# Kernel tuning notes

Measured on AMD Instinct MI355X. Metric: run time of the kernel, lower is better.

The kernel has to match this reference:

```python
import jax, jax.numpy as jnp
import numpy as np

INPUT_DIM = 512
HIDDEN_DIM = 512


def _linear_params(key, in_dim, out_dim):
    kw, kb = jax.random.split(key)
    bound = 1.0 / np.sqrt(in_dim)
    W = jax.random.uniform(kw, (out_dim, in_dim), minval=-bound, maxval=bound, dtype=jnp.float32)
    b = jax.random.uniform(kb, (out_dim,), minval=-bound, maxval=bound, dtype=jnp.float32)
    return W, b


def setup_inputs() -> dict:
    key = jax.random.key(0)
    keys = jax.random.split(key, 11)
    B = 8192
    inp = {
        "x_t": jax.random.normal(keys[0], (B, INPUT_DIM), dtype=jnp.float32),
        "h_tm1": jax.random.normal(keys[1], (B, HIDDEN_DIM), dtype=jnp.float32),
        "c_tm1": jax.random.normal(keys[2], (B, HIDDEN_DIM), dtype=jnp.float32),
    }
    names = ["f_x", "f_h", "i_x", "i_h", "g_x", "g_h", "o_x", "o_h"]
    for n, k in zip(names, keys[3:]):
        in_dim = INPUT_DIM if n.endswith("_x") else HIDDEN_DIM
        W, b = _linear_params(k, in_dim, HIDDEN_DIM)
        inp[f"W_{n}"] = W
        inp[f"b_{n}"] = b
    return inp


def reference(x_t, h_tm1, c_tm1,
              W_f_x, b_f_x, W_f_h, b_f_h,
              W_i_x, b_i_x, W_i_h, b_i_h,
              W_g_x, b_g_x, W_g_h, b_g_h,
              W_o_x, b_o_x, W_o_h, b_o_h):
    # Stacked weights: [4, H, D] -> einsum over D gives [B, 4, H].
    Wx = jnp.stack([W_f_x, W_g_x, W_i_x, W_o_x])  # [4, H, Din]
    bx = jnp.stack([b_f_x, b_g_x, b_i_x, b_o_x])  # [4, H]
    Wh = jnp.stack([W_f_h, W_g_h, W_i_h, W_o_h])
    bh = jnp.stack([b_f_h, b_g_h, b_i_h, b_o_h])
    pre = (jnp.einsum('bd,ghd->bgh', x_t, Wx) + bx
           + jnp.einsum('bd,ghd->bgh', h_tm1, Wh) + bh)  # [B, 4, H]
    f_t = jax.nn.sigmoid(pre[:, 0])
    g_t = jnp.tanh(pre[:, 1])
    i_t = jax.nn.sigmoid(pre[:, 2])
    o_t = jax.nn.sigmoid(pre[:, 3])
    c_t = f_t * c_tm1 + i_t * g_t
    h_t = o_t * jnp.tanh(c_t)
    return (h_t, c_t)
```

## Files before the change

kernel.cpp:

```cpp
#include <hip/hip_runtime.h>
#include <cstdint>
#include <cstddef>


typedef __attribute__((ext_vector_type(8))) short short8;
typedef __attribute__((ext_vector_type(4))) float floatx4;

#define AS1(p) ((const __attribute__((address_space(1))) void*)(p))
#define AS3(p) ((__attribute__((address_space(3))) void*)(p))

__device__ __forceinline__ unsigned short f2bf(float f) {
  union { float f; unsigned u; } v; v.f = f;
  unsigned u = v.u;
  return (unsigned short)((u + 0x7fffu + ((u >> 16) & 1u)) >> 16);
}

struct PackArgs {
  const float* x; const float* h;
  const float* wx[4]; const float* wh[4];
  const float* bx[4]; const float* bh[4];
  unsigned short* A; unsigned short* B; float* bias;
};

__global__ __launch_bounds__(256) void pack_all_kernel(PackArgs P) {
  const int bid = blockIdx.x;
  if (bid < 8192) {
    int e = (bid * 256 + threadIdx.x) * 4;
    int b = e >> 10, k = e & 1023;
    const float* src = (k < 512) ? (P.x + b * 512 + k)
                                 : (P.h + b * 512 + (k - 512));
    float4 v = *(const float4*)src;
    ushort4 o;
    o.x = f2bf(v.x); o.y = f2bf(v.y); o.z = f2bf(v.z); o.w = f2bf(v.w);
    *(ushort4*)(P.A + e) = o;
  } else {
    int e = ((bid - 8192) * 256 + threadIdx.x) * 4;
    int n = e >> 10, k = e & 1023;
    int g = n & 3, hh = n >> 2;
    const float* src = (k < 512) ? (P.wx[g] + hh * 512 + k)
                                 : (P.wh[g] + hh * 512 + (k - 512));
    float4 v = *(const float4*)src;
    ushort4 o;
    o.x = f2bf(v.x); o.y = f2bf(v.y); o.z = f2bf(v.z); o.w = f2bf(v.w);
    *(ushort4*)(P.B + e) = o;
    if (k == 0) P.bias[n] = P.bx[g][hh] + P.bh[g][hh];
  }
}

__global__ __launch_bounds__(256, 4)
void lstm_gemm_kernel(const unsigned short* __restrict__ A,
                      const unsigned short* __restrict__ B,
                      const float* __restrict__ bias,
                      const float* __restrict__ c_prev,
                      float* __restrict__ h_out,
                      float* __restrict__ c_out) {
  __shared__ __align__(16) char smem[33792];
  __shared__ __align__(16) float biasS[128];

  const int tid  = threadIdx.x;
  const int lane = tid & 63;
  const int w    = tid >> 6;
  const int quad = lane >> 4;
  const int colA = lane & 15;
  const int m0   = blockIdx.x * 128;
  const int n0   = blockIdx.y * 128;
  const int h0   = blockIdx.y * 32;

  if (tid < 128) biasS[tid] = bias[n0 + tid];

  const int wm = (w >> 1) * 64;
  const int wn = (w & 1) * 64;

  const int srow = tid >> 3;
  const int cl   = tid & 7;
  const int cg   = cl ^ (srow & 7);

  floatx4 acc[4][4];
#pragma unroll
  for (int i = 0; i < 4; ++i)
#pragma unroll
    for (int j = 0; j < 4; ++j) acc[i][j] = (floatx4){0.f, 0.f, 0.f, 0.f};

  const char* Ag = (const char*)A;
  const char* Bg = (const char*)B;

  for (int kt = 0; kt < 16; ++kt) {
    __syncthreads();
    const int kb = kt * 128;
#pragma unroll
    for (int j = 0; j < 4; ++j) {
      int r = j * 32 + srow;
      __builtin_amdgcn_global_load_lds(
          AS1(Ag + (size_t)(m0 + r) * 2048 + kb + cg * 16),
          AS3(smem + r * 128 + cl * 16), 16, 0, 0);
    }
#pragma unroll
    for (int j = 0; j < 4; ++j) {
      int r = j * 32 + srow;
      __builtin_amdgcn_global_load_lds(
          AS1(Bg + (size_t)(n0 + r) * 2048 + kb + cg * 16),
          AS3(smem + 16384 + r * 128 + cl * 16), 16, 0, 0);
    }
    __syncthreads();

#pragma unroll
    for (int kk = 0; kk < 2; ++kk) {
      const int off = ((kk * 4 + quad) ^ (colA & 7)) * 16;
      short8 af[4], bfr[4];
#pragma unroll
      for (int mi = 0; mi < 4; ++mi)
        af[mi] = *(const short8*)(smem + (wm + mi * 16 + colA) * 128 + off);
#pragma unroll
      for (int ni = 0; ni < 4; ++ni)
        bfr[ni] = *(const short8*)(smem + 16384 + (wn + ni * 16 + colA) * 128 + off);
#pragma unroll
      for (int mi = 0; mi < 4; ++mi)
#pragma unroll
        for (int ni = 0; ni < 4; ++ni)
          acc[mi][ni] = __builtin_amdgcn_mfma_f32_16x16x32_bf16(
              af[mi], bfr[ni], acc[mi][ni], 0, 0, 0);
    }
  }

  __syncthreads();
  float* ep = (float*)smem;
#pragma unroll
  for (int rd = 0; rd < 2; ++rd) {
    float cp[8];
#pragma unroll
    for (int j = 0; j < 8; ++j) {
      int idx  = j * 256 + tid;
      int mloc = idx >> 5;
      int hh   = idx & 31;
      cp[j] = c_prev[(m0 + rd * 64 + mloc) * 512 + h0 + hh];
    }
    if ((w >> 1) == rd) {
#pragma unroll
      for (int mi = 0; mi < 4; ++mi)
#pragma unroll
        for (int ni = 0; ni < 4; ++ni) {
          int rr0 = mi * 16 + quad * 4;
          int cc  = wn + ni * 16 + colA;
#pragma unroll
          for (int rr = 0; rr < 4; ++rr)
            ep[(rr0 + rr) * 132 + cc] = acc[mi][ni][rr];
        }
    }
    __syncthreads();
#pragma unroll
    for (int j = 0; j < 8; ++j) {
      int idx  = j * 256 + tid;
      int mloc = idx >> 5;
      int hh   = idx & 31;
      float4 pre = *(const float4*)(ep + mloc * 132 + hh * 4);
      float4 bb  = *(const float4*)(biasS + hh * 4);
      float pf = pre.x + bb.x;
      float pi = pre.y + bb.y;
      float pg = pre.z + bb.z;
      float po = pre.w + bb.w;
      float fg = 1.f / (1.f + __expf(-pf));
      float ig = 1.f / (1.f + __expf(-pi));
      float gg = 1.f - 2.f / (1.f + __expf(2.f * pg));
      float og = 1.f / (1.f + __expf(-po));
      float cv = fg * cp[j] + ig * gg;
      float th = 1.f - 2.f / (1.f + __expf(2.f * cv));
      int m  = m0 + rd * 64 + mloc;
      int hg = h0 + hh;
      h_out[m * 512 + hg] = og * th;
      c_out[m * 512 + hg] = cv;
    }
    __syncthreads();
  }
}

extern "C" void kernel_launch(void* const* d_in, const int* in_sizes, int n_in,
                              void* d_out, int out_size, void* d_ws, size_t ws_size,
                              hipStream_t stream) {
  char* ws = (char*)d_ws;
  unsigned short* Abf = (unsigned short*)ws;
  unsigned short* Bbf = (unsigned short*)(ws + (size_t)16777216);
  float* bias = (float*)(ws + (size_t)16777216 + 4194304);

  float* hout = (float*)d_out;
  float* cout = hout + (size_t)8192 * 512;

  PackArgs P;
  P.x = (const float*)d_in[0];
  P.h = (const float*)d_in[1];
  P.wx[0] = (const float*)d_in[3];  P.bx[0] = (const float*)d_in[4];
  P.wh[0] = (const float*)d_in[5];  P.bh[0] = (const float*)d_in[6];
  P.wx[1] = (const float*)d_in[7];  P.bx[1] = (const float*)d_in[8];
  P.wh[1] = (const float*)d_in[9];  P.bh[1] = (const float*)d_in[10];
  P.wx[2] = (const float*)d_in[11]; P.bx[2] = (const float*)d_in[12];
  P.wh[2] = (const float*)d_in[13]; P.bh[2] = (const float*)d_in[14];
  P.wx[3] = (const float*)d_in[15]; P.bx[3] = (const float*)d_in[16];
  P.wh[3] = (const float*)d_in[17]; P.bh[3] = (const float*)d_in[18];
  P.A = Abf; P.B = Bbf; P.bias = bias;

  pack_all_kernel<<<10240, 256, 0, stream>>>(P);

  const float* c = (const float*)d_in[2];
  dim3 grid(64, 16);
  lstm_gemm_kernel<<<grid, 256, 0, stream>>>(Abf, Bbf, bias, c, hout, cout);
}
```

Before: 170.4 us.

## Fuse activation bf16 conversion into GEMM, loading fp32 x/h directly into LDS

Drops the separate pass that converted x and h to a bf16 concatenated buffer. The GEMM now streams fp32 activations straight from x and h_in into LDS and converts them to bf16 in registers with v_cvt_pk_bf16_f32 before the MFMAs. The block tile grows to 256x128 with 512 threads and 80KB of LDS, and only the weights are still packed. This removes a 32MB read plus 16MB write round trip, but doubles A-tile LDS traffic, adds conversion ALU work in the inner loop, and may lower occupancy.

```diff
diff --git a/kernel.cpp b/kernel.cpp
--- a/kernel.cpp
+++ b/kernel.cpp
@@ -15,104 +15,106 @@
   return (unsigned short)((u + 0x7fffu + ((u >> 16) & 1u)) >> 16);
 }
 
-struct PackArgs {
-  const float* x; const float* h;
+struct PackBArgs {
   const float* wx[4]; const float* wh[4];
   const float* bx[4]; const float* bh[4];
-  unsigned short* A; unsigned short* B; float* bias;
+  unsigned short* B; float* bias;
 };
 
-__global__ __launch_bounds__(256) void pack_all_kernel(PackArgs P) {
-  const int bid = blockIdx.x;
-  if (bid < 8192) {
-    int e = (bid * 256 + threadIdx.x) * 4;
-    int b = e >> 10, k = e & 1023;
-    const float* src = (k < 512) ? (P.x + b * 512 + k)
-                                 : (P.h + b * 512 + (k - 512));
-    float4 v = *(const float4*)src;
-    ushort4 o;
-    o.x = f2bf(v.x); o.y = f2bf(v.y); o.z = f2bf(v.z); o.w = f2bf(v.w);
-    *(ushort4*)(P.A + e) = o;
-  } else {
-    int e = ((bid - 8192) * 256 + threadIdx.x) * 4;
-    int n = e >> 10, k = e & 1023;
-    int g = n & 3, hh = n >> 2;
-    const float* src = (k < 512) ? (P.wx[g] + hh * 512 + k)
-                                 : (P.wh[g] + hh * 512 + (k - 512));
-    float4 v = *(const float4*)src;
-    ushort4 o;
-    o.x = f2bf(v.x); o.y = f2bf(v.y); o.z = f2bf(v.z); o.w = f2bf(v.w);
-    *(ushort4*)(P.B + e) = o;
-    if (k == 0) P.bias[n] = P.bx[g][hh] + P.bh[g][hh];
-  }
-}
-
-__global__ __launch_bounds__(256, 4)
-void lstm_gemm_kernel(const unsigned short* __restrict__ A,
+__global__ __launch_bounds__(256) void pack_b_kernel(PackBArgs P) {
+  const int n  = blockIdx.x;
+  const int g  = n & 3, hh = n >> 2;
+  const int k  = threadIdx.x * 4;
+  const float* src = (k < 512) ? (P.wx[g] + hh * 512 + k)
+                               : (P.wh[g] + hh * 512 + (k - 512));
+  float4 v = *(const float4*)src;
+  ushort4 o;
+  o.x = f2bf(v.x); o.y = f2bf(v.y); o.z = f2bf(v.z); o.w = f2bf(v.w);
+  *(ushort4*)(P.B + n * 1024 + k) = o;
+  if (threadIdx.x == 0) P.bias[n] = P.bx[g][hh] + P.bh[g][hh];
+}
+
+__global__ __launch_bounds__(512, 4)
+void lstm_gemm_kernel(const float* __restrict__ x,
+                      const float* __restrict__ h_in,
                       const unsigned short* __restrict__ B,
                       const float* __restrict__ bias,
                       const float* __restrict__ c_prev,
                       float* __restrict__ h_out,
                       float* __restrict__ c_out) {
-  __shared__ __align__(16) char smem[33792];
-  __shared__ __align__(16) float biasS[128];
+  __shared__ __align__(16) char smem[81920];
 
   const int tid  = threadIdx.x;
   const int lane = tid & 63;
   const int w    = tid >> 6;
   const int quad = lane >> 4;
   const int colA = lane & 15;
-  const int m0   = blockIdx.x * 128;
+  const int m0   = blockIdx.x * 256;
   const int n0   = blockIdx.y * 128;
   const int h0   = blockIdx.y * 32;
 
-  if (tid < 128) biasS[tid] = bias[n0 + tid];
-
   const int wm = (w >> 1) * 64;
   const int wn = (w & 1) * 64;
 
+  const int aRow = tid >> 4;
+  const int aSwz = ((tid & 15) ^ (aRow & 15)) * 16;
   const int srow = tid >> 3;
   const int cl   = tid & 7;
   const int cg   = cl ^ (srow & 7);
 
+  const char* Bg = (const char*)B;
+
   floatx4 acc[4][4];
 #pragma unroll
   for (int i = 0; i < 4; ++i)
 #pragma unroll
     for (int j = 0; j < 4; ++j) acc[i][j] = (floatx4){0.f, 0.f, 0.f, 0.f};
 
-  const char* Ag = (const char*)A;
-  const char* Bg = (const char*)B;
-
   for (int kt = 0; kt < 16; ++kt) {
     __syncthreads();
-    const int kb = kt * 128;
-#pragma unroll
-    for (int j = 0; j < 4; ++j) {
-      int r = j * 32 + srow;
+    const char* Asrc = (const char*)((kt < 8) ? x : h_in);
+    const size_t kbA = (size_t)((kt & 7) * 256);
+    const int    kbB = kt * 128;
+#pragma unroll
+    for (int j = 0; j < 8; ++j) {
+      int r = j * 32 + aRow;
       __builtin_amdgcn_global_load_lds(
-          AS1(Ag + (size_t)(m0 + r) * 2048 + kb + cg * 16),
-          AS3(smem + r * 128 + cl * 16), 16, 0, 0);
-    }
-#pragma unroll
-    for (int j = 0; j < 4; ++j) {
-      int r = j * 32 + srow;
+          AS1(Asrc + (size_t)(m0 + r) * 2048 + kbA + aSwz),
+          AS3(smem + j * 8192 + tid * 16), 16, 0, 0);
+    }
+#pragma unroll
+    for (int j = 0; j < 2; ++j) {
+      int r = j * 64 + srow;
       __builtin_amdgcn_global_load_lds(
-          AS1(Bg + (size_t)(n0 + r) * 2048 + kb + cg * 16),
-          AS3(smem + 16384 + r * 128 + cl * 16), 16, 0, 0);
+          AS1(Bg + (size_t)(n0 + r) * 2048 + kbB + cg * 16),
+          AS3(smem + 65536 + j * 8192 + tid * 16), 16, 0, 0);
     }
     __syncthreads();
 
 #pragma unroll
     for (int kk = 0; kk < 2; ++kk) {
-      const int off = ((kk * 4 + quad) ^ (colA & 7)) * 16;
-      short8 af[4], bfr[4];
-#pragma unroll
-      for (int mi = 0; mi < 4; ++mi)
-        af[mi] = *(const short8*)(smem + (wm + mi * 16 + colA) * 128 + off);
+      const int e0   = kk * 8 + quad * 2;
+      const int offA = (e0 ^ colA) * 16;
+      short8 af[4];
+#pragma unroll
+      for (int mi = 0; mi < 4; ++mi) {
+        const char* pa = smem + (wm + mi * 16 + colA) * 256;
+        floatx4 lo = *(const floatx4*)(pa + offA);
+        floatx4 hi = *(const floatx4*)(pa + (offA ^ 16));
+        unsigned q0, q1, q2, q3;
+        asm("v_cvt_pk_bf16_f32 %0, %1, %2" : "=v"(q0) : "v"(lo[0]), "v"(lo[1]));
+        asm("v_cvt_pk_bf16_f32 %0, %1, %2" : "=v"(q1) : "v"(lo[2]), "v"(lo[3]));
+        asm("v_cvt_pk_bf16_f32 %0, %1, %2" : "=v"(q2) : "v"(hi[0]), "v"(hi[1]));
+        asm("v_cvt_pk_bf16_f32 %0, %1, %2" : "=v"(q3) : "v"(hi[2]), "v"(hi[3]));
+        union { unsigned u[4]; short8 s; } cv;
+        cv.u[0] = q0; cv.u[1] = q1; cv.u[2] = q2; cv.u[3] = q3;
+        af[mi] = cv.s;
+      }
+      const int offB = ((kk * 4 + quad) ^ (colA & 7)) * 16;
+      short8 bfr[4];
 #pragma unroll
       for (int ni = 0; ni < 4; ++ni)
-        bfr[ni] = *(const short8*)(smem + 16384 + (wn + ni * 16 + colA) * 128 + off);
+        bfr[ni] = *(const short8*)(smem + 65536 + (wn + ni * 16 + colA) * 128 + offB);
 #pragma unroll
       for (int mi = 0; mi < 4; ++mi)
 #pragma unroll
@@ -123,13 +125,15 @@
   }
 
   __syncthreads();
-  float* ep = (float*)smem;
-#pragma unroll
-  for (int rd = 0; rd < 2; ++rd) {
-    float cp[8];
-#pragma unroll
-    for (int j = 0; j < 8; ++j) {
-      int idx  = j * 256 + tid;
+  float* ep    = (float*)smem;
+  float* biasE = (float*)(smem + 33792);
+  if (tid < 128) biasE[tid] = bias[n0 + tid];
+#pragma unroll
+  for (int rd = 0; rd < 4; ++rd) {
+    float cp[4];
+#pragma unroll
+    for (int j = 0; j < 4; ++j) {
+      int idx  = j * 512 + tid;
       int mloc = idx >> 5;
       int hh   = idx & 31;
       cp[j] = c_prev[(m0 + rd * 64 + mloc) * 512 + h0 + hh];
@@ -148,12 +152,12 @@
     }
     __syncthreads();
 #pragma unroll
-    for (int j = 0; j < 8; ++j) {
-      int idx  = j * 256 + tid;
+    for (int j = 0; j < 4; ++j) {
+      int idx  = j * 512 + tid;
       int mloc = idx >> 5;
       int hh   = idx & 31;
       float4 pre = *(const float4*)(ep + mloc * 132 + hh * 4);
-      float4 bb  = *(const float4*)(biasS + hh * 4);
+      float4 bb  = *(const float4*)(biasE + hh * 4);
       float pf = pre.x + bb.x;
       float pi = pre.y + bb.y;
       float pg = pre.z + bb.z;
@@ -177,16 +181,13 @@
                               void* d_out, int out_size, void* d_ws, size_t ws_size,
                               hipStream_t stream) {
   char* ws = (char*)d_ws;
-  unsigned short* Abf = (unsigned short*)ws;
-  unsigned short* Bbf = (unsigned short*)(ws + (size_t)16777216);
-  float* bias = (float*)(ws + (size_t)16777216 + 4194304);
+  unsigned short* Bbf = (unsigned short*)ws;
+  float* bias = (float*)(ws + (size_t)4194304);
 
   float* hout = (float*)d_out;
   float* cout = hout + (size_t)8192 * 512;
 
-  PackArgs P;
-  P.x = (const float*)d_in[0];
-  P.h = (const float*)d_in[1];
+  PackBArgs P;
   P.wx[0] = (const float*)d_in[3];  P.bx[0] = (const float*)d_in[4];
   P.wh[0] = (const float*)d_in[5];  P.bh[0] = (const float*)d_in[6];
   P.wx[1] = (const float*)d_in[7];  P.bx[1] = (const float*)d_in[8];
@@ -195,11 +196,13 @@
   P.wh[2] = (const float*)d_in[13]; P.bh[2] = (const float*)d_in[14];
   P.wx[3] = (const float*)d_in[15]; P.bx[3] = (const float*)d_in[16];
   P.wh[3] = (const float*)d_in[17]; P.bh[3] = (const float*)d_in[18];
-  P.A = Abf; P.B = Bbf; P.bias = bias;
-
-  pack_all_kernel<<<10240, 256, 0, stream>>>(P);
-
-  const float* c = (const float*)d_in[2];
-  dim3 grid(64, 16);
-  lstm_gemm_kernel<<<grid, 256, 0, stream>>>(Abf, Bbf, bias, c, hout, cout);
-}
+  P.B = Bbf; P.bias = bias;
+
+  pack_b_kernel<<<2048, 256, 0, stream>>>(P);
+
+  const float* xin = (const float*)d_in[0];
+  const float* hin = (const float*)d_in[1];
+  const float* c   = (const float*)d_in[2];
+  dim3 grid(32, 16);
+  lstm_gemm_kernel<<<grid, 512, 0, stream>>>(xin, hin, Bbf, bias, c, hout, cout);
+}
```

Result: slower. 174.0 us (+2.1%).

## Pre-tile operands into MFMA fragment layout and load directly to registers

Applied to the files above, without the earlier changes.

The pack kernel now writes A and B in a 16-row tile layout that matches the MFMA fragment order, with each thread converting 8 elements. The GEMM drops the LDS staging and barriers and loads fragments straight from global memory into registers, double-buffered across k-steps. This removes the shared-memory round trip and synchronisation, but each operand is now read from global memory or L2 by every wave that uses it instead of once per block. Register pressure also rises, so launch bounds drop to 2 blocks per CU.

```diff
diff --git a/kernel.cpp b/kernel.cpp
--- a/kernel.cpp
+++ b/kernel.cpp
@@ -5,9 +5,6 @@
 
 typedef __attribute__((ext_vector_type(8))) short short8;
 typedef __attribute__((ext_vector_type(4))) float floatx4;
-
-#define AS1(p) ((const __attribute__((address_space(1))) void*)(p))
-#define AS3(p) ((__attribute__((address_space(3))) void*)(p))
 
 __device__ __forceinline__ unsigned short f2bf(float f) {
   union { float f; unsigned u; } v; v.f = f;
@@ -22,39 +19,75 @@
   unsigned short* A; unsigned short* B; float* bias;
 };
 
-__global__ __launch_bounds__(256) void pack_all_kernel(PackArgs P) {
-  const int bid = blockIdx.x;
-  if (bid < 8192) {
-    int e = (bid * 256 + threadIdx.x) * 4;
-    int b = e >> 10, k = e & 1023;
-    const float* src = (k < 512) ? (P.x + b * 512 + k)
-                                 : (P.h + b * 512 + (k - 512));
-    float4 v = *(const float4*)src;
-    ushort4 o;
-    o.x = f2bf(v.x); o.y = f2bf(v.y); o.z = f2bf(v.z); o.w = f2bf(v.w);
-    *(ushort4*)(P.A + e) = o;
+__global__ __launch_bounds__(256) void pack_kernel(PackArgs P) {
+  const int gid = blockIdx.x * 256 + threadIdx.x;
+  if (blockIdx.x < 4096) {
+    int g  = gid;
+    int r  = g & 15, c = (g >> 4) & 7, kt = (g >> 7) & 15, mt = g >> 11;
+    int m  = mt * 16 + r;
+    int k  = kt * 64 + c * 8;
+    const float* src = (k < 512) ? (P.x + m * 512 + k)
+                                 : (P.h + m * 512 + (k - 512));
+    float4 v0 = ((const float4*)src)[0];
+    float4 v1 = ((const float4*)src)[1];
+    union { unsigned short us[8]; short8 s; } o;
+    o.us[0] = f2bf(v0.x); o.us[1] = f2bf(v0.y);
+    o.us[2] = f2bf(v0.z); o.us[3] = f2bf(v0.w);
+    o.us[4] = f2bf(v1.x); o.us[5] = f2bf(v1.y);
+    o.us[6] = f2bf(v1.z); o.us[7] = f2bf(v1.w);
+    *(short8*)(P.A + (size_t)g * 8) = o.s;
   } else {
-    int e = ((bid - 8192) * 256 + threadIdx.x) * 4;
-    int n = e >> 10, k = e & 1023;
-    int g = n & 3, hh = n >> 2;
-    const float* src = (k < 512) ? (P.wx[g] + hh * 512 + k)
-                                 : (P.wh[g] + hh * 512 + (k - 512));
-    float4 v = *(const float4*)src;
-    ushort4 o;
-    o.x = f2bf(v.x); o.y = f2bf(v.y); o.z = f2bf(v.z); o.w = f2bf(v.w);
-    *(ushort4*)(P.B + e) = o;
-    if (k == 0) P.bias[n] = P.bx[g][hh] + P.bh[g][hh];
+    int g  = gid - 4096 * 256;
+    int r  = g & 15, c = (g >> 4) & 7, kt = (g >> 7) & 15, nt = g >> 11;
+    int n  = nt * 16 + r;
+    int gate = n & 3, hh = n >> 2;
+    int k  = kt * 64 + c * 8;
+    const float* src = (k < 512) ? (P.wx[gate] + hh * 512 + k)
+                                 : (P.wh[gate] + hh * 512 + (k - 512));
+    float4 v0 = ((const float4*)src)[0];
+    float4 v1 = ((const float4*)src)[1];
+    union { unsigned short us[8]; short8 s; } o;
+    o.us[0] = f2bf(v0.x); o.us[1] = f2bf(v0.y);
+    o.us[2] = f2bf(v0.z); o.us[3] = f2bf(v0.w);
+    o.us[4] = f2bf(v1.x); o.us[5] = f2bf(v1.y);
+    o.us[6] = f2bf(v1.z); o.us[7] = f2bf(v1.w);
+    *(short8*)(P.B + (size_t)g * 8) = o.s;
+    if (kt == 0 && c == 0) P.bias[n] = P.bx[gate][hh] + P.bh[gate][hh];
   }
 }
 
-__global__ __launch_bounds__(256, 4)
+#define LOADK(AF, BF, KT) do {                                            \
+    _Pragma("unroll")                                                     \
+    for (int mi_ = 0; mi_ < 4; ++mi_) {                                   \
+      AF[mi_][0] = *(const short8*)(Aw + mi_ * 16384 + (KT) * 1024 + loff);        \
+      AF[mi_][1] = *(const short8*)(Aw + mi_ * 16384 + (KT) * 1024 + 512 + loff);  \
+    }                                                                     \
+    _Pragma("unroll")                                                     \
+    for (int ni_ = 0; ni_ < 4; ++ni_) {                                   \
+      BF[ni_][0] = *(const short8*)(Bw + ni_ * 16384 + (KT) * 1024 + loff);        \
+      BF[ni_][1] = *(const short8*)(Bw + ni_ * 16384 + (KT) * 1024 + 512 + loff);  \
+    }                                                                     \
+  } while (0)
+
+#define MFMA_ALL(AF, BF) do {                                             \
+    _Pragma("unroll")                                                     \
+    for (int mi_ = 0; mi_ < 4; ++mi_)                                     \
+      _Pragma("unroll")                                                   \
+      for (int ni_ = 0; ni_ < 4; ++ni_)                                   \
+        _Pragma("unroll")                                                 \
+        for (int kk_ = 0; kk_ < 2; ++kk_)                                 \
+          acc[mi_][ni_] = __builtin_amdgcn_mfma_f32_16x16x32_bf16(        \
+              AF[mi_][kk_], BF[ni_][kk_], acc[mi_][ni_], 0, 0, 0);        \
+  } while (0)
+
+__global__ __launch_bounds__(256, 2)
 void lstm_gemm_kernel(const unsigned short* __restrict__ A,
                       const unsigned short* __restrict__ B,
                       const float* __restrict__ bias,
                       const float* __restrict__ c_prev,
                       float* __restrict__ h_out,
                       float* __restrict__ c_out) {
-  __shared__ __align__(16) char smem[33792];
+  __shared__ __align__(16) float ep[64 * 132];
   __shared__ __align__(16) float biasS[128];
 
   const int tid  = threadIdx.x;
@@ -71,9 +104,9 @@
   const int wm = (w >> 1) * 64;
   const int wn = (w & 1) * 64;
 
-  const int srow = tid >> 3;
-  const int cl   = tid & 7;
-  const int cg   = cl ^ (srow & 7);
+  const unsigned short* Aw = A + (size_t)(blockIdx.x * 8 + (w >> 1) * 4) * 16384;
+  const unsigned short* Bw = B + (size_t)(blockIdx.y * 8 + (w & 1) * 4) * 16384;
+  const int loff = quad * 128 + colA * 8;
 
   floatx4 acc[4][4];
 #pragma unroll
@@ -81,49 +114,17 @@
 #pragma unroll
     for (int j = 0; j < 4; ++j) acc[i][j] = (floatx4){0.f, 0.f, 0.f, 0.f};
 
-  const char* Ag = (const char*)A;
-  const char* Bg = (const char*)B;
-
-  for (int kt = 0; kt < 16; ++kt) {
-    __syncthreads();
-    const int kb = kt * 128;
-#pragma unroll
-    for (int j = 0; j < 4; ++j) {
-      int r = j * 32 + srow;
-      __builtin_amdgcn_global_load_lds(
-          AS1(Ag + (size_t)(m0 + r) * 2048 + kb + cg * 16),
-          AS3(smem + r * 128 + cl * 16), 16, 0, 0);
-    }
-#pragma unroll
-    for (int j = 0; j < 4; ++j) {
-      int r = j * 32 + srow;
-      __builtin_amdgcn_global_load_lds(
-          AS1(Bg + (size_t)(n0 + r) * 2048 + kb + cg * 16),
-          AS3(smem + 16384 + r * 128 + cl * 16), 16, 0, 0);
-    }
-    __syncthreads();
-
-#pragma unroll
-    for (int kk = 0; kk < 2; ++kk) {
-      const int off = ((kk * 4 + quad) ^ (colA & 7)) * 16;
-      short8 af[4], bfr[4];
-#pragma unroll
-      for (int mi = 0; mi < 4; ++mi)
-        af[mi] = *(const short8*)(smem + (wm + mi * 16 + colA) * 128 + off);
-#pragma unroll
-      for (int ni = 0; ni < 4; ++ni)
-        bfr[ni] = *(const short8*)(smem + 16384 + (wn + ni * 16 + colA) * 128 + off);
-#pragma unroll
-      for (int mi = 0; mi < 4; ++mi)
-#pragma unroll
-        for (int ni = 0; ni < 4; ++ni)
-          acc[mi][ni] = __builtin_amdgcn_mfma_f32_16x16x32_bf16(
-              af[mi], bfr[ni], acc[mi][ni], 0, 0, 0);
-    }
+  short8 a0[4][2], b0[4][2], a1[4][2], b1[4][2];
+  LOADK(a0, b0, 0);
+#pragma unroll
+  for (int kt = 0; kt < 16; kt += 2) {
+    LOADK(a1, b1, kt + 1);
+    MFMA_ALL(a0, b0);
+    if (kt + 2 < 16) LOADK(a0, b0, kt + 2);
+    MFMA_ALL(a1, b1);
   }
 
   __syncthreads();
-  float* ep = (float*)smem;
 #pragma unroll
   for (int rd = 0; rd < 2; ++rd) {
     float cp[8];
@@ -197,7 +198,7 @@
   P.wh[3] = (const float*)d_in[17]; P.bh[3] = (const float*)d_in[18];
   P.A = Abf; P.B = Bbf; P.bias = bias;
 
-  pack_all_kernel<<<10240, 256, 0, stream>>>(P);
+  pack_kernel<<<5120, 256, 0, stream>>>(P);
 
   const float* c = (const float*)d_in[2];
   dim3 grid(64, 16);
```

Result: slower. 197.3 us (+15.8%).
